# Performance work log

Measured on AMD Instinct MI355X. Metric: run time of the kernel, lower is better.

Reference implementation:

```python
import jax, jax.numpy as jnp
import numpy as np

N_NODES = 100000
N_EDGES = 1000000
D_NODE = 64
D_EDGE = 32
D_OUT = 64
EPS = 1e-07
BETA = 1.0


def setup_inputs() -> dict:
    key = jax.random.key(0)
    ks = jax.random.split(key, 6)
    node_feats = jax.random.normal(ks[0], (N_NODES, D_NODE), dtype=jnp.float32)
    edge_feats = jax.random.normal(ks[1], (N_EDGES, D_EDGE), dtype=jnp.float32)
    src = jax.random.randint(ks[2], (N_EDGES,), 0, N_NODES, dtype=jnp.int32)
    dst = jax.random.randint(ks[3], (N_EDGES,), 0, N_NODES, dtype=jnp.int32)
    We = jax.random.normal(ks[4], (D_EDGE, D_OUT), dtype=jnp.float32) / np.sqrt(D_EDGE)
    be = jnp.zeros((D_OUT,), dtype=jnp.float32)
    Wm = jax.random.normal(ks[5], (D_NODE, D_OUT), dtype=jnp.float32) / np.sqrt(D_NODE)
    bm = jnp.zeros((D_OUT,), dtype=jnp.float32)
    return {"node_feats": node_feats, "edge_feats": edge_feats, "src": src,
            "dst": dst, "We": We, "be": be, "Wm": Wm, "bm": bm}


def reference(node_feats, edge_feats, src, dst, We, be, Wm, bm):
    n = node_feats.shape[0]
    # edge encoder + u_add_e: m_e = h_src + Linear(e)
    m = node_feats[src] + (edge_feats @ We + be)          # [E, D]
    m = jax.nn.relu(m) + EPS
    # segmented (per-destination) softmax over edges, per feature channel
    z = m * BETA
    zmax = jax.ops.segment_max(z, dst, num_segments=n)    # [N, D]
    ez = jnp.exp(z - zmax[dst])                           # [E, D]
    denom = jax.ops.segment_sum(ez, dst, num_segments=n)  # [N, D]
    a = ez / denom[dst]                                   # [E, D]
    # weighted scatter-sum aggregation
    agg = jax.ops.segment_sum(m * a, dst, num_segments=n) # [N, D]
    feats = node_feats + agg
    # mlp_layers=1 -> single Linear
    return feats @ Wm + bm
```

## Files before the change

kernel.cpp:

```cpp
#include <hip/hip_runtime.h>
#include <hip/hip_bf16.h>

#define D_NODE 64
#define D_EDGE 32
#define D_OUT  64
#define EPSF   1e-7f
#define CAP    64

__global__ __launch_bounds__(256) void genconv_build_kernel(
    const int* __restrict__ src,
    const int* __restrict__ dst,
    int* __restrict__ cnt,
    int2* __restrict__ slots,
    int E)
{
    const int e = blockIdx.x * blockDim.x + threadIdx.x;
    if (e >= E) return;
    const int d = dst[e];
    const int pos = atomicAdd(&cnt[d], 1);
    if (pos < CAP)
        slots[(size_t)d * CAP + pos] = make_int2(e, src[e]);
}

__global__ __launch_bounds__(256) void genconv_gather_kernel(
    const float* __restrict__ node,
    const float* __restrict__ ef,
    const int* __restrict__ cnt,
    const int2* __restrict__ slots,
    const float* __restrict__ We,
    const float* __restrict__ be,
    const float* __restrict__ Wm,
    const float* __restrict__ bm,
    float* __restrict__ out,
    int N)
{
    __shared__ float wm_s[D_NODE * D_OUT];
    __shared__ __align__(16) float fbuf[4][D_NODE];
    for (int i = threadIdx.x; i < D_NODE * D_OUT; i += blockDim.x)
        wm_s[i] = Wm[i];
    __syncthreads();

    const int lane  = threadIdx.x & 63;
    const int wslot = threadIdx.x >> 6;

    float w[D_EDGE];
#pragma unroll
    for (int k = 0; k < D_EDGE; ++k)
        w[k] = We[k * D_OUT + lane];
    const float bias_e = be[lane];
    const float bias_m = bm[lane];

    const int wid = (int)((blockIdx.x * blockDim.x + threadIdx.x) >> 6);
    const int nw  = (int)((gridDim.x * blockDim.x) >> 6);

    for (int n = wid; n < N; n += nw) {
        const size_t base = (size_t)n * D_NODE;
        const int c = min(cnt[n], CAP);
        const int2* sl = slots + (size_t)n * CAP;

        float fres = node[base + lane];
        float num = 0.0f, den = 0.0f;

        int i = 0;
        for (; i + 1 < c; i += 2) {
            const int2 p0 = sl[i];
            const int2 p1 = sl[i + 1];
            const int e0 = __builtin_amdgcn_readfirstlane(p0.x);
            const int s0 = __builtin_amdgcn_readfirstlane(p0.y);
            const int e1 = __builtin_amdgcn_readfirstlane(p1.x);
            const int s1 = __builtin_amdgcn_readfirstlane(p1.y);

            const float* ep0 = ef + (size_t)e0 * D_EDGE;
            const float* ep1 = ef + (size_t)e1 * D_EDGE;
            const float h0 = node[(size_t)s0 * D_NODE + lane];
            const float h1 = node[(size_t)s1 * D_NODE + lane];

            float v0 = bias_e, v1 = bias_e;
#pragma unroll
            for (int k = 0; k < D_EDGE; ++k) {
                v0 = fmaf(ep0[k], w[k], v0);
                v1 = fmaf(ep1[k], w[k], v1);
            }
            const float m0 = fmaxf(h0 + v0, 0.0f) + EPSF;
            const float m1 = fmaxf(h1 + v1, 0.0f) + EPSF;
            const float z0 = __expf(m0);
            const float z1 = __expf(m1);
            num = fmaf(m0, z0, num);
            num = fmaf(m1, z1, num);
            den += z0;
            den += z1;
        }
        if (i < c) {
            const int2 p0 = sl[i];
            const int e0 = __builtin_amdgcn_readfirstlane(p0.x);
            const int s0 = __builtin_amdgcn_readfirstlane(p0.y);
            const float* ep0 = ef + (size_t)e0 * D_EDGE;
            const float h0 = node[(size_t)s0 * D_NODE + lane];
            float v0 = bias_e;
#pragma unroll
            for (int k = 0; k < D_EDGE; ++k)
                v0 = fmaf(ep0[k], w[k], v0);
            const float m0 = fmaxf(h0 + v0, 0.0f) + EPSF;
            const float z0 = __expf(m0);
            num = fmaf(m0, z0, num);
            den += z0;
        }

        float f = fres;
        if (c > 0)
            f += num / den;

        fbuf[wslot][lane] = f;
        float acc = bias_m;
#pragma unroll
        for (int d4 = 0; d4 < D_NODE / 4; ++d4) {
            const float4 fv = *(const float4*)&fbuf[wslot][d4 * 4];
            acc = fmaf(fv.x, wm_s[(d4 * 4 + 0) * D_OUT + lane], acc);
            acc = fmaf(fv.y, wm_s[(d4 * 4 + 1) * D_OUT + lane], acc);
            acc = fmaf(fv.z, wm_s[(d4 * 4 + 2) * D_OUT + lane], acc);
            acc = fmaf(fv.w, wm_s[(d4 * 4 + 3) * D_OUT + lane], acc);
        }
        out[base + lane] = acc;
    }
}

extern "C" void kernel_launch(void* const* d_in, const int* in_sizes, int n_in,
                              void* d_out, int out_size, void* d_ws, size_t ws_size,
                              hipStream_t stream)
{
    const float* node = (const float*)d_in[0];
    const float* ef   = (const float*)d_in[1];
    const int*   src  = (const int*)d_in[2];
    const int*   dst  = (const int*)d_in[3];
    const float* We   = (const float*)d_in[4];
    const float* be   = (const float*)d_in[5];
    const float* Wm   = (const float*)d_in[6];
    const float* bm   = (const float*)d_in[7];
    float* out = (float*)d_out;

    const int N = in_sizes[0] / D_NODE;
    const int E = in_sizes[2];

    int*  cnt   = (int*)d_ws;
    int2* slots = (int2*)(cnt + N);

    hipMemsetAsync(cnt, 0, (size_t)N * sizeof(int), stream);

    genconv_build_kernel<<<(E + 255) / 256, 256, 0, stream>>>(src, dst, cnt, slots, E);

    genconv_gather_kernel<<<2048, 256, 0, stream>>>(node, ef, cnt, slots,
                                                    We, be, Wm, bm, out, N);
}
```

Before: 446.2 us.

## Software-pipeline edge gathers via LDS staging and shrink slot table to edge ids

The build kernel now stores only edge ids (int instead of int2), processes four edges per thread, and the slot capacity drops from 64 to 48. The gather kernel loads a node's whole slot list in one coalesced wave read, looks up src per lane, and broadcasts ids with readlane. It double-buffers edge feature rows through shared memory so the next pair's loads overlap the current pair's compute, and it prefetches the next node's count, slots and residual. Lowering CAP risks truncating high in-degree nodes, though random degree around 10 makes overflow unlikely, and the extra shared-memory staging adds LDS traffic.

```diff
diff --git a/kernel.cpp b/kernel.cpp
--- a/kernel.cpp
+++ b/kernel.cpp
@@ -1,32 +1,47 @@
 #include <hip/hip_runtime.h>
-#include <hip/hip_bf16.h>
 
 #define D_NODE 64
 #define D_EDGE 32
 #define D_OUT  64
 #define EPSF   1e-7f
-#define CAP    64
+#define CAP    48
 
 __global__ __launch_bounds__(256) void genconv_build_kernel(
-    const int* __restrict__ src,
     const int* __restrict__ dst,
     int* __restrict__ cnt,
-    int2* __restrict__ slots,
+    int* __restrict__ slots,
     int E)
 {
-    const int e = blockIdx.x * blockDim.x + threadIdx.x;
-    if (e >= E) return;
-    const int d = dst[e];
-    const int pos = atomicAdd(&cnt[d], 1);
-    if (pos < CAP)
-        slots[(size_t)d * CAP + pos] = make_int2(e, src[e]);
+    const int stride = (int)(gridDim.x * blockDim.x);
+    int e = (int)(blockIdx.x * blockDim.x + threadIdx.x);
+    for (; e + 3 * stride < E; e += 4 * stride) {
+        const int e0 = e, e1 = e + stride, e2 = e + 2 * stride, e3 = e + 3 * stride;
+        const int d0 = dst[e0];
+        const int d1 = dst[e1];
+        const int d2 = dst[e2];
+        const int d3 = dst[e3];
+        const int p0 = atomicAdd(&cnt[d0], 1);
+        const int p1 = atomicAdd(&cnt[d1], 1);
+        const int p2 = atomicAdd(&cnt[d2], 1);
+        const int p3 = atomicAdd(&cnt[d3], 1);
+        if (p0 < CAP) slots[d0 * CAP + p0] = e0;
+        if (p1 < CAP) slots[d1 * CAP + p1] = e1;
+        if (p2 < CAP) slots[d2 * CAP + p2] = e2;
+        if (p3 < CAP) slots[d3 * CAP + p3] = e3;
+    }
+    for (; e < E; e += stride) {
+        const int d = dst[e];
+        const int pos = atomicAdd(&cnt[d], 1);
+        if (pos < CAP) slots[d * CAP + pos] = e;
+    }
 }
 
 __global__ __launch_bounds__(256) void genconv_gather_kernel(
     const float* __restrict__ node,
     const float* __restrict__ ef,
-    const int* __restrict__ cnt,
-    const int2* __restrict__ slots,
+    const int*   __restrict__ srcv,
+    const int*   __restrict__ cnt,
+    const int*   __restrict__ slots,
     const float* __restrict__ We,
     const float* __restrict__ be,
     const float* __restrict__ Wm,
@@ -35,13 +50,15 @@
     int N)
 {
     __shared__ float wm_s[D_NODE * D_OUT];
+    __shared__ __align__(16) float ef_s[4][2][64];
     __shared__ __align__(16) float fbuf[4][D_NODE];
+
     for (int i = threadIdx.x; i < D_NODE * D_OUT; i += blockDim.x)
         wm_s[i] = Wm[i];
     __syncthreads();
 
-    const int lane  = threadIdx.x & 63;
-    const int wslot = threadIdx.x >> 6;
+    const int lane  = (int)(threadIdx.x & 63);
+    const int wslot = (int)(threadIdx.x >> 6);
 
     float w[D_EDGE];
 #pragma unroll
@@ -53,57 +70,99 @@
     const int wid = (int)((blockIdx.x * blockDim.x + threadIdx.x) >> 6);
     const int nw  = (int)((gridDim.x * blockDim.x) >> 6);
 
-    for (int n = wid; n < N; n += nw) {
-        const size_t base = (size_t)n * D_NODE;
-        const int c = min(cnt[n], CAP);
-        const int2* sl = slots + (size_t)n * CAP;
-
-        float fres = node[base + lane];
+    float* const efA = ef_s[wslot][0];
+    float* const efB = ef_s[wslot][1];
+
+    int n = wid;
+    int   c_pf = 0, slot_pf = 0;
+    float res_pf = 0.0f;
+    if (n < N) {
+        c_pf    = cnt[n];
+        slot_pf = (lane < CAP) ? slots[n * CAP + lane] : 0;
+        res_pf  = node[(size_t)n * D_NODE + lane];
+    }
+
+    while (n < N) {
+        const int   c      = min(c_pf, CAP);
+        const int   slot_v = slot_pf;
+        const float fres   = res_pf;
+
+        const int n_next = n + nw;
+        if (n_next < N) {
+            c_pf    = cnt[n_next];
+            slot_pf = (lane < CAP) ? slots[n_next * CAP + lane] : 0;
+            res_pf  = node[(size_t)n_next * D_NODE + lane];
+        }
+
+        const int e_l = (lane < c) ? slot_v : 0;
+        const int s_l = srcv[e_l];
+
         float num = 0.0f, den = 0.0f;
 
-        int i = 0;
-        for (; i + 1 < c; i += 2) {
-            const int2 p0 = sl[i];
-            const int2 p1 = sl[i + 1];
-            const int e0 = __builtin_amdgcn_readfirstlane(p0.x);
-            const int s0 = __builtin_amdgcn_readfirstlane(p0.y);
-            const int e1 = __builtin_amdgcn_readfirstlane(p1.x);
-            const int s1 = __builtin_amdgcn_readfirstlane(p1.y);
-
-            const float* ep0 = ef + (size_t)e0 * D_EDGE;
-            const float* ep1 = ef + (size_t)e1 * D_EDGE;
-            const float h0 = node[(size_t)s0 * D_NODE + lane];
-            const float h1 = node[(size_t)s1 * D_NODE + lane];
-
+        const int npairs = (c + 1) >> 1;
+
+        float efvA = 0.f, h0A = 0.f, h1A = 0.f; int i1vA = 0;
+        float efvB = 0.f, h0B = 0.f, h1B = 0.f; int i1vB = 0;
+
+        auto stage = [&](int p, float& efv, float& h0, float& h1, int& i1v) {
+            const int i0  = 2 * p;
+            const int i1  = 2 * p + 1;
+            i1v = (i1 < c);
+            const int i1c = i1v ? i1 : i0;
+            const int e0  = __builtin_amdgcn_readlane(e_l, i0);
+            const int e1  = __builtin_amdgcn_readlane(e_l, i1c);
+            const int s0  = __builtin_amdgcn_readlane(s_l, i0);
+            const int s1  = __builtin_amdgcn_readlane(s_l, i1c);
+            const int er  = (lane < 32) ? e0 : e1;
+            efv = ef[(size_t)er * D_EDGE + (lane & 31)];
+            h0  = node[(size_t)s0 * D_NODE + lane];
+            h1  = node[(size_t)s1 * D_NODE + lane];
+        };
+
+        auto compute = [&](const float* eb, float h0, float h1, int i1v) {
             float v0 = bias_e, v1 = bias_e;
 #pragma unroll
-            for (int k = 0; k < D_EDGE; ++k) {
-                v0 = fmaf(ep0[k], w[k], v0);
-                v1 = fmaf(ep1[k], w[k], v1);
+            for (int k4 = 0; k4 < D_EDGE / 4; ++k4) {
+                const float4 a0 = *(const float4*)(eb + k4 * 4);
+                const float4 a1 = *(const float4*)(eb + 32 + k4 * 4);
+                v0 = fmaf(a0.x, w[4 * k4 + 0], v0);
+                v0 = fmaf(a0.y, w[4 * k4 + 1], v0);
+                v0 = fmaf(a0.z, w[4 * k4 + 2], v0);
+                v0 = fmaf(a0.w, w[4 * k4 + 3], v0);
+                v1 = fmaf(a1.x, w[4 * k4 + 0], v1);
+                v1 = fmaf(a1.y, w[4 * k4 + 1], v1);
+                v1 = fmaf(a1.z, w[4 * k4 + 2], v1);
+                v1 = fmaf(a1.w, w[4 * k4 + 3], v1);
             }
-            const float m0 = fmaxf(h0 + v0, 0.0f) + EPSF;
-            const float m1 = fmaxf(h1 + v1, 0.0f) + EPSF;
-            const float z0 = __expf(m0);
-            const float z1 = __expf(m1);
-            num = fmaf(m0, z0, num);
-            num = fmaf(m1, z1, num);
-            den += z0;
-            den += z1;
-        }
-        if (i < c) {
-            const int2 p0 = sl[i];
-            const int e0 = __builtin_amdgcn_readfirstlane(p0.x);
-            const int s0 = __builtin_amdgcn_readfirstlane(p0.y);
-            const float* ep0 = ef + (size_t)e0 * D_EDGE;
-            const float h0 = node[(size_t)s0 * D_NODE + lane];
-            float v0 = bias_e;
-#pragma unroll
-            for (int k = 0; k < D_EDGE; ++k)
-                v0 = fmaf(ep0[k], w[k], v0);
             const float m0 = fmaxf(h0 + v0, 0.0f) + EPSF;
             const float z0 = __expf(m0);
             num = fmaf(m0, z0, num);
             den += z0;
+            if (i1v) {
+                const float m1 = fmaxf(h1 + v1, 0.0f) + EPSF;
+                const float z1 = __expf(m1);
+                num = fmaf(m1, z1, num);
+                den += z1;
+            }
+        };
+
+        if (npairs > 0) {
+            stage(0, efvA, h0A, h1A, i1vA);
+            efA[lane] = efvA;
+            if (npairs > 1) stage(1, efvB, h0B, h1B, i1vB);
+            int p = 0;
+            for (;;) {
+                compute(efA, h0A, h1A, i1vA);
+                ++p;
+                if (p >= npairs) break;
+                efB[lane] = efvB;
+                if (p + 1 < npairs) stage(p + 1, efvA, h0A, h1A, i1vA);
+                compute(efB, h0B, h1B, i1vB);
+                ++p;
+                if (p >= npairs) break;
+                efA[lane] = efvA;
+                if (p + 1 < npairs) stage(p + 1, efvB, h0B, h1B, i1vB);
+            }
         }
 
         float f = fres;
@@ -120,7 +179,9 @@
             acc = fmaf(fv.z, wm_s[(d4 * 4 + 2) * D_OUT + lane], acc);
             acc = fmaf(fv.w, wm_s[(d4 * 4 + 3) * D_OUT + lane], acc);
         }
-        out[base + lane] = acc;
+        out[(size_t)n * D_NODE + lane] = acc;
+
+        n = n_next;
     }
 }
 
@@ -141,13 +202,14 @@
     const int N = in_sizes[0] / D_NODE;
     const int E = in_sizes[2];
 
-    int*  cnt   = (int*)d_ws;
-    int2* slots = (int2*)(cnt + N);
+    int* cnt   = (int*)d_ws;
+    int* slots = cnt + N;
 
     hipMemsetAsync(cnt, 0, (size_t)N * sizeof(int), stream);
 
-    genconv_build_kernel<<<(E + 255) / 256, 256, 0, stream>>>(src, dst, cnt, slots, E);
-
-    genconv_gather_kernel<<<2048, 256, 0, stream>>>(node, ef, cnt, slots,
+    const int bblk = (E + 1023) >> 10;
+    genconv_build_kernel<<<bblk, 256, 0, stream>>>(dst, cnt, slots, E);
+
+    genconv_gather_kernel<<<2048, 256, 0, stream>>>(node, ef, src, cnt, slots,
                                                     We, be, Wm, bm, out, N);
 }
```

New measurement: 527.9 us. 1.18x slower.

## Prefetch next node's slot list into lanes and unroll edge loop by four

Applied to the files above, without the earlier changes.

The gather kernel now loads the whole slot list for a node with one coalesced per-lane load and pulls edge and source indices out with readlane, where before it did serial scalar loads per edge. It also prefetches the next node's count, slots and residual features during the current node, and unrolls the edge loop to four edges at a time for more memory-level parallelism. CAP is reduced to 48 so the slot list fits in a wavefront. Nodes with more than 48 incoming edges are now truncated, which is possible given an average in-degree of 10 but unlikely. The extra registers may lower occupancy.

```diff
diff --git a/kernel.cpp b/kernel.cpp
--- a/kernel.cpp
+++ b/kernel.cpp
@@ -1,11 +1,10 @@
 #include <hip/hip_runtime.h>
-#include <hip/hip_bf16.h>
 
 #define D_NODE 64
 #define D_EDGE 32
 #define D_OUT  64
 #define EPSF   1e-7f
-#define CAP    64
+#define CAP    48
 
 __global__ __launch_bounds__(256) void genconv_build_kernel(
     const int* __restrict__ src,
@@ -19,13 +18,13 @@
     const int d = dst[e];
     const int pos = atomicAdd(&cnt[d], 1);
     if (pos < CAP)
-        slots[(size_t)d * CAP + pos] = make_int2(e, src[e]);
+        slots[d * CAP + pos] = make_int2(e, src[e]);
 }
 
 __global__ __launch_bounds__(256) void genconv_gather_kernel(
     const float* __restrict__ node,
     const float* __restrict__ ef,
-    const int* __restrict__ cnt,
+    const int*  __restrict__ cnt,
     const int2* __restrict__ slots,
     const float* __restrict__ We,
     const float* __restrict__ be,
@@ -36,12 +35,13 @@
 {
     __shared__ float wm_s[D_NODE * D_OUT];
     __shared__ __align__(16) float fbuf[4][D_NODE];
+
     for (int i = threadIdx.x; i < D_NODE * D_OUT; i += blockDim.x)
         wm_s[i] = Wm[i];
     __syncthreads();
 
-    const int lane  = threadIdx.x & 63;
-    const int wslot = threadIdx.x >> 6;
+    const int lane  = (int)(threadIdx.x & 63);
+    const int wslot = (int)(threadIdx.x >> 6);
 
     float w[D_EDGE];
 #pragma unroll
@@ -53,47 +53,77 @@
     const int wid = (int)((blockIdx.x * blockDim.x + threadIdx.x) >> 6);
     const int nw  = (int)((gridDim.x * blockDim.x) >> 6);
 
-    for (int n = wid; n < N; n += nw) {
-        const size_t base = (size_t)n * D_NODE;
-        const int c = min(cnt[n], CAP);
-        const int2* sl = slots + (size_t)n * CAP;
+    int n = wid;
+    int   c_pf   = 0;
+    int2  sl_pf  = make_int2(0, 0);
+    float res_pf = 0.0f;
+    if (n < N) {
+        c_pf   = cnt[n];
+        sl_pf  = (lane < CAP) ? slots[n * CAP + lane] : make_int2(0, 0);
+        res_pf = node[(size_t)n * D_NODE + lane];
+    }
 
-        float fres = node[base + lane];
+    while (n < N) {
+        const int   c    = min(c_pf, CAP);
+        const int   e_l  = sl_pf.x;
+        const int   s_l  = sl_pf.y;
+        const float fres = res_pf;
+
+        const int n_next = n + nw;
+        if (n_next < N) {
+            c_pf   = cnt[n_next];
+            sl_pf  = (lane < CAP) ? slots[n_next * CAP + lane] : make_int2(0, 0);
+            res_pf = node[(size_t)n_next * D_NODE + lane];
+        }
+
         float num = 0.0f, den = 0.0f;
 
         int i = 0;
-        for (; i + 1 < c; i += 2) {
-            const int2 p0 = sl[i];
-            const int2 p1 = sl[i + 1];
-            const int e0 = __builtin_amdgcn_readfirstlane(p0.x);
-            const int s0 = __builtin_amdgcn_readfirstlane(p0.y);
-            const int e1 = __builtin_amdgcn_readfirstlane(p1.x);
-            const int s1 = __builtin_amdgcn_readfirstlane(p1.y);
+        for (; i + 3 < c; i += 4) {
+            const int e0 = __builtin_amdgcn_readlane(e_l, i + 0);
+            const int s0 = __builtin_amdgcn_readlane(s_l, i + 0);
+            const int e1 = __builtin_amdgcn_readlane(e_l, i + 1);
+            const int s1 = __builtin_amdgcn_readlane(s_l, i + 1);
+            const int e2 = __builtin_amdgcn_readlane(e_l, i + 2);
+            const int s2 = __builtin_amdgcn_readlane(s_l, i + 2);
+            const int e3 = __builtin_amdgcn_readlane(e_l, i + 3);
+            const int s3 = __builtin_amdgcn_readlane(s_l, i + 3);
 
             const float* ep0 = ef + (size_t)e0 * D_EDGE;
             const float* ep1 = ef + (size_t)e1 * D_EDGE;
+            const float* ep2 = ef + (size_t)e2 * D_EDGE;
+            const float* ep3 = ef + (size_t)e3 * D_EDGE;
             const float h0 = node[(size_t)s0 * D_NODE + lane];
             const float h1 = node[(size_t)s1 * D_NODE + lane];
+            const float h2 = node[(size_t)s2 * D_NODE + lane];
+            const float h3 = node[(size_t)s3 * D_NODE + lane];
 
-            float v0 = bias_e, v1 = bias_e;
+            float v0 = bias_e, v1 = bias_e, v2 = bias_e, v3 = bias_e;
 #pragma unroll
             for (int k = 0; k < D_EDGE; ++k) {
                 v0 = fmaf(ep0[k], w[k], v0);
                 v1 = fmaf(ep1[k], w[k], v1);
+                v2 = fmaf(ep2[k], w[k], v2);
+                v3 = fmaf(ep3[k], w[k], v3);
             }
             const float m0 = fmaxf(h0 + v0, 0.0f) + EPSF;
             const float m1 = fmaxf(h1 + v1, 0.0f) + EPSF;
+            const float m2 = fmaxf(h2 + v2, 0.0f) + EPSF;
+            const float m3 = fmaxf(h3 + v3, 0.0f) + EPSF;
             const float z0 = __expf(m0);
             const float z1 = __expf(m1);
+            const float z2 = __expf(m2);
+            const float z3 = __expf(m3);
             num = fmaf(m0, z0, num);
             num = fmaf(m1, z1, num);
-            den += z0;
-            den += z1;
+            num = fmaf(m2, z2, num);
+            num = fmaf(m3, z3, num);
+            den += z0 + z1;
+            den += z2 + z3;
         }
-        if (i < c) {
-            const int2 p0 = sl[i];
-            const int e0 = __builtin_amdgcn_readfirstlane(p0.x);
-            const int s0 = __builtin_amdgcn_readfirstlane(p0.y);
+        for (; i < c; ++i) {
+            const int e0 = __builtin_amdgcn_readlane(e_l, i);
+            const int s0 = __builtin_amdgcn_readlane(s_l, i);
             const float* ep0 = ef + (size_t)e0 * D_EDGE;
             const float h0 = node[(size_t)s0 * D_NODE + lane];
             float v0 = bias_e;
@@ -120,7 +150,9 @@
             acc = fmaf(fv.z, wm_s[(d4 * 4 + 2) * D_OUT + lane], acc);
             acc = fmaf(fv.w, wm_s[(d4 * 4 + 3) * D_OUT + lane], acc);
         }
-        out[base + lane] = acc;
+        out[(size_t)n * D_NODE + lane] = acc;
+
+        n = n_next;
     }
 }
 
```

Result: slower. 491.6 us (+10.2%).
